# Kernel optimization log

Measured on AMD Instinct MI355X. Metric: run time of the kernel, lower is better.

Reference implementation:

```python
import jax, jax.numpy as jnp
import numpy as np

EPS = 1e-5

def _bn(x, g, b, m, v):
    # eval-mode batchnorm, NCHW, per-channel params
    inv = g / jnp.sqrt(v + EPS)
    return x * inv[None, :, None, None] + (b - m * inv)[None, :, None, None]

def setup_inputs() -> dict:
    key = jax.random.key(0)
    ks = jax.random.split(key, 16)
    C = 64
    x = jax.random.normal(ks[0], (8, C, 64, 64), dtype=jnp.float32)
    w1 = jax.random.normal(ks[1], (C, C, 1, 1), dtype=jnp.float32) * 0.1
    w2 = jax.random.normal(ks[2], (C, 1, 3, 3), dtype=jnp.float32) * 0.1
    w3 = jax.random.normal(ks[3], (C, C, 1, 1), dtype=jnp.float32) * 0.1
    def bn_params(k):
        k1, k2, k3, k4 = jax.random.split(k, 4)
        return (jax.random.uniform(k1, (C,)) + 0.5,
                jax.random.normal(k2, (C,)) * 0.1,
                jax.random.normal(k3, (C,)) * 0.1,
                jax.random.uniform(k4, (C,)) + 0.5)
    g1, b1, m1, v1 = bn_params(ks[4])
    g2, b2, m2, v2 = bn_params(ks[5])
    g3, b3, m3, v3 = bn_params(ks[6])
    return {"x": x, "w1": w1, "bn1_g": g1, "bn1_b": b1, "bn1_m": m1, "bn1_v": v1,
            "w2": w2, "bn2_g": g2, "bn2_b": b2, "bn2_m": m2, "bn2_v": v2,
            "w3": w3, "bn3_g": g3, "bn3_b": b3, "bn3_m": m3, "bn3_v": v3}

def reference(x, w1, bn1_g, bn1_b, bn1_m, bn1_v,
              w2, bn2_g, bn2_b, bn2_m, bn2_v,
              w3, bn3_g, bn3_b, bn3_m, bn3_v):
    B, c, h, w = x.shape
    N = h * w
    # conv1 (1x1) + BN + ReLU -> V
    v = jnp.einsum('bchw,oc->bohw', x, w1[:, :, 0, 0])
    v = jax.nn.relu(_bn(v, bn1_g, bn1_b, bn1_m, bn1_v))
    # attention over spatial positions: Q=K=x, single head, dim=c
    Q = x.reshape(B, c, N)          # bdn
    V = v.reshape(B, c, N)          # bdm
    scores = jnp.einsum('bdn,bdm->bnm', Q, Q) / (c ** 0.5)  # [B,N,N]
    prob = jax.nn.softmax(scores, axis=-1)
    out = jnp.einsum('bnm,bdm->bdn', prob, V).reshape(B, c, h, w)
    # depthwise conv + BN + ReLU
    out = jax.lax.conv_general_dilated(
        out, w2, window_strides=(1, 1), padding='SAME',
        dimension_numbers=('NCHW', 'OIHW', 'NCHW'), feature_group_count=c)
    out = jax.nn.relu(_bn(out, bn2_g, bn2_b, bn2_m, bn2_v))
    # pointwise conv + BN
    out = jnp.einsum('bchw,oc->bohw', out, w3[:, :, 0, 0])
    out = _bn(out, bn3_g, bn3_b, bn3_m, bn3_v)
    # residual (stride==1 and in_size==out_size)
    return out + x
```

## Files before the change

### kernel.cpp

```cpp
#include <hip/hip_runtime.h>
#include <stdint.h>

typedef __attribute__((ext_vector_type(8)))  short s16x8;
typedef __attribute__((ext_vector_type(16))) float f32x16;

union CvtI4 { int4 i; s16x8 s; };

__device__ __forceinline__ unsigned f2bf(float f) {
    union { float f; unsigned u; } v; v.f = f;
    return (v.u + 0x7fffu + ((v.u >> 16) & 1u)) >> 16;
}

__global__ __launch_bounds__(256) void k_prep(
    const float* __restrict__ x, const float* __restrict__ w1,
    const float* __restrict__ g1, const float* __restrict__ b1,
    const float* __restrict__ m1, const float* __restrict__ v1,
    unsigned short* __restrict__ xT, unsigned short* __restrict__ vbf)
{
    __shared__ float X[64 * 65];
    const int b    = blockIdx.x >> 7;
    const int n0   = ((blockIdx.x >> 1) & 63) << 6;
    const int half = blockIdx.x & 1;
    const int tid  = threadIdx.x;
    const float QS = 0.42466090014400953f;

    {
        const int r = tid >> 6, nn = tid & 63;
        const float* xb = x + (size_t)b * 262144 + n0 + nn;
#pragma unroll
        for (int cc = 0; cc < 16; ++cc) {
            int c = cc * 4 + r;
            X[c * 65 + nn] = xb[(size_t)c * 4096];
        }
    }
    __syncthreads();

    {
        const int n8 = tid >> 3, c8 = tid & 7;
        const int n = (half << 5) + n8;
        unsigned u[4];
#pragma unroll
        for (int j = 0; j < 4; ++j) {
            unsigned lo = f2bf(X[(c8 * 8 + 2 * j) * 65 + n] * QS);
            unsigned hi = f2bf(X[(c8 * 8 + 2 * j + 1) * 65 + n] * QS);
            u[j] = lo | (hi << 16);
        }
        uint4 pk; pk.x = u[0]; pk.y = u[1]; pk.z = u[2]; pk.w = u[3];
        *(uint4*)(xT + (((size_t)((b << 12) + n0 + n)) << 6) + (c8 << 3)) = pk;
    }

    {
        const int n = tid & 63, og = tid >> 6;
        float rX[64];
#pragma unroll
        for (int c = 0; c < 64; ++c) rX[c] = X[c * 65 + n];
        unsigned short* vb = vbf + (((size_t)(b << 6)) << 12) + n0 + n;
#pragma unroll 2
        for (int oo = 0; oo < 8; ++oo) {
            int o = (half << 5) + og * 8 + oo;
            float inv = g1[o] * rsqrtf(v1[o] + 1e-5f);
            float sh  = b1[o] - m1[o] * inv;
            float acc = 0.f;
#pragma unroll
            for (int c = 0; c < 64; ++c) acc = fmaf(w1[o * 64 + c], rX[c], acc);
            vb[(size_t)o << 12] = (unsigned short)f2bf(fmaxf(fmaf(acc, inv, sh), 0.f));
        }
    }
}

__global__ __launch_bounds__(512) void k_attn(
    const unsigned short* __restrict__ xT, const unsigned short* __restrict__ vbf,
    unsigned short* __restrict__ outO)
{
    __shared__ __align__(16) unsigned short Klds[2][64 * 64];
    __shared__ __align__(16) unsigned short Vlds[2][64 * 64];
    __shared__ __align__(16) unsigned short Plds[2][64 * 64];
    __shared__ float rsLds[4][32];
    __shared__ float denomT[64];

    const int b    = blockIdx.x & 7;
    const int qgrp = blockIdx.x >> 3;
    const int tid  = threadIdx.x;
    const int w = tid >> 6, lane = tid & 63;
    const int l31 = lane & 31, half = lane >> 5;
    const int qbase = qgrp << 6;
    const int T = 64;

    const bool isQK = (w < 4);
    const int wr = isQK ? w : (w - 4);
    const int s = wr & 1;
    const int t = wr >> 1;

    s16x8 Bq[4];
    float rs = 0.f;
    const int kr0 = (tid & 255) >> 3, c4 = tid & 7;
    const int kr1 = kr0 + 32;
    const size_t kOff0 = (((size_t)((b << 12) + kr0)) << 6) + (c4 << 3);
    const size_t kOff1 = (((size_t)((b << 12) + kr1)) << 6) + (c4 << 3);
    const int kx0 = (c4 ^ (kr0 & 7)) << 3, kx1 = (c4 ^ (kr1 & 7)) << 3;
    const size_t vOff0 = (((size_t)((b << 6) + kr0)) << 12) + (c4 << 3);
    const size_t vOff1 = (((size_t)((b << 6) + kr1)) << 12) + (c4 << 3);

    int4 kpre0, kpre1, vpre0, vpre1;

    f32x16 O = {0.f,0.f,0.f,0.f,0.f,0.f,0.f,0.f,0.f,0.f,0.f,0.f,0.f,0.f,0.f,0.f};

    if (isQK) {
        const unsigned short* qr = xT +
            (((size_t)((b << 12) + qbase + (t << 5) + l31)) << 6) + (half << 3);
#pragma unroll
        for (int kk = 0; kk < 4; ++kk) {
            CvtI4 c; c.i = *(const int4*)(qr + (kk << 4));
            Bq[kk] = c.s;
        }
        {
            int4 a0 = *(const int4*)(xT + kOff0);
            int4 a1 = *(const int4*)(xT + kOff1);
            *(int4*)(Klds[0] + (kr0 << 6) + kx0) = a0;
            *(int4*)(Klds[0] + (kr1 << 6) + kx1) = a1;
            a0 = *(const int4*)(xT + kOff0 + ((size_t)1 << 12));
            a1 = *(const int4*)(xT + kOff1 + ((size_t)1 << 12));
            *(int4*)(Klds[1] + (kr0 << 6) + kx0) = a0;
            *(int4*)(Klds[1] + (kr1 << 6) + kx1) = a1;
            kpre0 = *(const int4*)(xT + kOff0 + ((size_t)2 << 12));
            kpre1 = *(const int4*)(xT + kOff1 + ((size_t)2 << 12));
        }
    } else {
        int4 a0 = *(const int4*)(vbf + vOff0);
        int4 a1 = *(const int4*)(vbf + vOff1);
        *(int4*)(Vlds[0] + (kr0 << 6) + kx0) = a0;
        *(int4*)(Vlds[0] + (kr1 << 6) + kx1) = a1;
        vpre0 = *(const int4*)(vbf + vOff0 + (1 << 6));
        vpre1 = *(const int4*)(vbf + vOff1 + (1 << 6));
    }
    __syncthreads();

    if (isQK) {
        const int km = (s << 5) + l31;
        s16x8 Ak[4];
#pragma unroll
        for (int kk = 0; kk < 4; ++kk)
            Ak[kk] = *(const s16x8*)(Klds[0] + (km << 6) + ((((kk << 1) + half) ^ (km & 7)) << 3));
        f32x16 S = {0.f,0.f,0.f,0.f,0.f,0.f,0.f,0.f,0.f,0.f,0.f,0.f,0.f,0.f,0.f,0.f};
        S = __builtin_amdgcn_mfma_f32_32x32x16_bf16(Ak[0], Bq[0], S, 0, 0, 0);
        S = __builtin_amdgcn_mfma_f32_32x32x16_bf16(Ak[1], Bq[1], S, 0, 0, 0);
        S = __builtin_amdgcn_mfma_f32_32x32x16_bf16(Ak[2], Bq[2], S, 0, 0, 0);
        S = __builtin_amdgcn_mfma_f32_32x32x16_bf16(Ak[3], Bq[3], S, 0, 0, 0);
        const int nrow = (t << 5) + l31;
#pragma unroll
        for (int q = 0; q < 4; ++q) {
            float p0 = __builtin_amdgcn_exp2f(S[4*q+0]);
            float p1 = __builtin_amdgcn_exp2f(S[4*q+1]);
            float p2 = __builtin_amdgcn_exp2f(S[4*q+2]);
            float p3 = __builtin_amdgcn_exp2f(S[4*q+3]);
            rs += (p0 + p1) + (p2 + p3);
            union { float f; unsigned u; } a0, a1, a2, a3;
            a0.f = p0; a1.f = p1; a2.f = p2; a3.f = p3;
            uint2 pk;
            pk.x = __builtin_amdgcn_perm(a1.u + 0x8000u, a0.u + 0x8000u, 0x07060302u);
            pk.y = __builtin_amdgcn_perm(a3.u + 0x8000u, a2.u + 0x8000u, 0x07060302u);
            int c8 = (s << 2) + q;
            *(uint2*)(Plds[0] + (nrow << 6) + ((c8 ^ (nrow & 7)) << 3) + (half << 2)) = pk;
        }
    }
    __syncthreads();

    for (int i = 0; i < T; ++i) {
        if (isQK) {
            *(int4*)(Klds[i & 1] + (kr0 << 6) + kx0) = kpre0;
            *(int4*)(Klds[i & 1] + (kr1 << 6) + kx1) = kpre1;
            {
                size_t tk = (size_t)((i + 3 < T) ? (i + 3) : (T - 1)) << 12;
                kpre0 = *(const int4*)(xT + kOff0 + tk);
                kpre1 = *(const int4*)(xT + kOff1 + tk);
            }
            if (i + 1 < T) {
                const int km = (s << 5) + l31;
                const unsigned short* Kb = Klds[(i + 1) & 1];
                s16x8 Ak[4];
#pragma unroll
                for (int kk = 0; kk < 4; ++kk)
                    Ak[kk] = *(const s16x8*)(Kb + (km << 6) + ((((kk << 1) + half) ^ (km & 7)) << 3));
                f32x16 S = {0.f,0.f,0.f,0.f,0.f,0.f,0.f,0.f,0.f,0.f,0.f,0.f,0.f,0.f,0.f,0.f};
                S = __builtin_amdgcn_mfma_f32_32x32x16_bf16(Ak[0], Bq[0], S, 0, 0, 0);
                S = __builtin_amdgcn_mfma_f32_32x32x16_bf16(Ak[1], Bq[1], S, 0, 0, 0);
                S = __builtin_amdgcn_mfma_f32_32x32x16_bf16(Ak[2], Bq[2], S, 0, 0, 0);
                S = __builtin_amdgcn_mfma_f32_32x32x16_bf16(Ak[3], Bq[3], S, 0, 0, 0);
                const int nrow = (t << 5) + l31;
                unsigned short* Pb = Plds[(i + 1) & 1];
#pragma unroll
                for (int q = 0; q < 4; ++q) {
                    float p0 = __builtin_amdgcn_exp2f(S[4*q+0]);
                    float p1 = __builtin_amdgcn_exp2f(S[4*q+1]);
                    float p2 = __builtin_amdgcn_exp2f(S[4*q+2]);
                    float p3 = __builtin_amdgcn_exp2f(S[4*q+3]);
                    rs += (p0 + p1) + (p2 + p3);
                    union { float f; unsigned u; } a0, a1, a2, a3;
                    a0.f = p0; a1.f = p1; a2.f = p2; a3.f = p3;
                    uint2 pk;
                    pk.x = __builtin_amdgcn_perm(a1.u + 0x8000u, a0.u + 0x8000u, 0x07060302u);
                    pk.y = __builtin_amdgcn_perm(a3.u + 0x8000u, a2.u + 0x8000u, 0x07060302u);
                    int c8 = (s << 2) + q;
                    *(uint2*)(Pb + (nrow << 6) + ((c8 ^ (nrow & 7)) << 3) + (half << 2)) = pk;
                }
            }
        } else {
            *(int4*)(Vlds[(i + 1) & 1] + (kr0 << 6) + kx0) = vpre0;
            *(int4*)(Vlds[(i + 1) & 1] + (kr1 << 6) + kx1) = vpre1;
            {
                int tv = ((i + 2 < T) ? (i + 2) : (T - 1)) << 6;
                vpre0 = *(const int4*)(vbf + vOff0 + tv);
                vpre1 = *(const int4*)(vbf + vOff1 + tv);
            }
            const int nrow = (t << 5) + l31;
            const int drow = (s << 5) + l31;
            const unsigned short* Pb = Plds[i & 1];
            const unsigned short* Vb = Vlds[i & 1];
#pragma unroll
            for (int ks = 0; ks < 4; ++ks) {
                int c = (ks << 1) + half;
                const s16x8 Ap = *(const s16x8*)(Pb + (nrow << 6) + ((c ^ (nrow & 7)) << 3));
                const s16x8 Bv = *(const s16x8*)(Vb + (drow << 6) + ((c ^ (drow & 7)) << 3));
                O = __builtin_amdgcn_mfma_f32_32x32x16_bf16(Ap, Bv, O, 0, 0, 0);
            }
        }
        __syncthreads();
    }

    if (isQK) {
        rs += __shfl_xor(rs, 32);
        if (half == 0) rsLds[w][l31] = rs;
    }
    __syncthreads();
    if (tid < 64) {
        int tt = tid >> 5, n = tid & 31;
        denomT[tid] = rsLds[2 * tt][n] + rsLds[2 * tt + 1][n];
    }
    __syncthreads();

    if (!isQK) {
        const int nb = (b << 12) + qbase;
#pragma unroll
        for (int r = 0; r < 16; ++r) {
            int nl = (r & 3) + ((r >> 2) << 3) + (half << 2);
            int n = (t << 5) + nl;
            float inv = 1.f / denomT[n];
            outO[((size_t)(nb + n) << 6) + (s << 5) + l31] = (unsigned short)f2bf(O[r] * inv);
        }
    }
}

__global__ __launch_bounds__(256) void k_post(
    const unsigned short* __restrict__ Obase,
    const float* __restrict__ x,
    const float* __restrict__ w2,
    const float* __restrict__ g2, const float* __restrict__ b2,
    const float* __restrict__ m2, const float* __restrict__ v2,
    const float* __restrict__ w3,
    const float* __restrict__ g3, const float* __restrict__ b3,
    const float* __restrict__ m3, const float* __restrict__ v3,
    float* __restrict__ out)
{
    __shared__ float W[3][64 * 66];
    __shared__ float T2[64 * 66];

    const int b = blockIdx.x >> 6;
    const int h = blockIdx.x & 63;
    const int tid = threadIdx.x;

#pragma unroll
    for (int r = 0; r < 3; ++r) {
        int hh = h + r - 1;
        if (hh >= 0 && hh <= 63) {
#pragma unroll
            for (int i = 0; i < 2; ++i) {
                int lin = (i << 8) + tid;
                int w = lin >> 3, cg = lin & 7;
                size_t npos = (size_t)((b << 12) + (hh << 6) + w);
                uint4 v = *(const uint4*)(Obase + (npos << 6) + (cg << 3));
                float* Wd = &W[r][w * 66 + (cg << 3)];
                union { float f; unsigned u; } t;
                t.u = v.x << 16;         Wd[0] = t.f;
                t.u = v.x & 0xFFFF0000u; Wd[1] = t.f;
                t.u = v.y << 16;         Wd[2] = t.f;
                t.u = v.y & 0xFFFF0000u; Wd[3] = t.f;
                t.u = v.z << 16;         Wd[4] = t.f;
                t.u = v.z & 0xFFFF0000u; Wd[5] = t.f;
                t.u = v.w << 16;         Wd[6] = t.f;
                t.u = v.w & 0xFFFF0000u; Wd[7] = t.f;
            }
        } else {
#pragma unroll
            for (int i = 0; i < 2; ++i) {
                int lin = (i << 8) + tid;
                float* Wd = &W[r][(lin >> 3) * 66 + ((lin & 7) << 3)];
#pragma unroll
                for (int j = 0; j < 8; ++j) Wd[j] = 0.f;
            }
        }
    }
    __syncthreads();

    const int w = tid & 63, cq = tid >> 6;
    float t16[16];
#pragma unroll
    for (int i = 0; i < 16; ++i) t16[i] = 0.f;

#pragma unroll
    for (int ky = 0; ky < 3; ++ky) {
#pragma unroll
        for (int kx = 0; kx < 3; ++kx) {
            int ww = w + kx - 1;
            if (ww < 0 || ww > 63) continue;
            const int k = ky * 3 + kx;
            const float* Wr = &W[ky][ww * 66 + (cq << 4)];
#pragma unroll
            for (int i = 0; i < 4; ++i) {
                float4 a = *(const float4*)(Wr + (i << 2));
                int c = (cq << 4) + (i << 2);
                t16[i * 4 + 0] = fmaf(w2[(c + 0) * 9 + k], a.x, t16[i * 4 + 0]);
                t16[i * 4 + 1] = fmaf(w2[(c + 1) * 9 + k], a.y, t16[i * 4 + 1]);
                t16[i * 4 + 2] = fmaf(w2[(c + 2) * 9 + k], a.z, t16[i * 4 + 2]);
                t16[i * 4 + 3] = fmaf(w2[(c + 3) * 9 + k], a.w, t16[i * 4 + 3]);
            }
        }
    }
#pragma unroll
    for (int i = 0; i < 16; ++i) {
        int c = (cq << 4) + i;
        float inv = g2[c] * rsqrtf(v2[c] + 1e-5f);
        float sh  = b2[c] - m2[c] * inv;
        T2[w * 66 + c] = fmaxf(fmaf(t16[i], inv, sh), 0.f);
    }
    __syncthreads();

    float rT[64];
#pragma unroll
    for (int c4 = 0; c4 < 16; ++c4)
        *(float4*)&rT[c4 << 2] = *(const float4*)&T2[w * 66 + (c4 << 2)];

    const int hw = (h << 6) + w;
#pragma unroll 2
    for (int oo = 0; oo < 16; ++oo) {
        int o = (cq << 4) + oo;
        float inv = g3[o] * rsqrtf(v3[o] + 1e-5f);
        float sh  = b3[o] - m3[o] * inv;
        float acc = 0.f;
#pragma unroll
        for (int c = 0; c < 64; ++c) acc = fmaf(w3[o * 64 + c], rT[c], acc);
        size_t idx = (((size_t)((b << 6) + o)) << 12) + hw;
        out[idx] = fmaf(acc, inv, sh) + x[idx];
    }
}

extern "C" void kernel_launch(void* const* d_in, const int* in_sizes, int n_in,
                              void* d_out, int out_size, void* d_ws, size_t ws_size,
                              hipStream_t stream)
{
    const float* x  = (const float*)d_in[0];
    const float* w1 = (const float*)d_in[1];
    const float* g1 = (const float*)d_in[2];
    const float* b1 = (const float*)d_in[3];
    const float* m1 = (const float*)d_in[4];
    const float* v1 = (const float*)d_in[5];
    const float* w2 = (const float*)d_in[6];
    const float* g2 = (const float*)d_in[7];
    const float* b2 = (const float*)d_in[8];
    const float* m2 = (const float*)d_in[9];
    const float* v2 = (const float*)d_in[10];
    const float* w3 = (const float*)d_in[11];
    const float* g3 = (const float*)d_in[12];
    const float* b3 = (const float*)d_in[13];
    const float* m3 = (const float*)d_in[14];
    const float* v3 = (const float*)d_in[15];
    float* out = (float*)d_out;

    unsigned short* xT  = (unsigned short*)d_ws;
    unsigned short* vbf = xT + (size_t)8 * 4096 * 64;
    unsigned short* Obase = (unsigned short*)((char*)d_ws + (8u << 20));

    k_prep<<<1024, 256, 0, stream>>>(x, w1, g1, b1, m1, v1, xT, vbf);
    k_attn<<<512, 512, 0, stream>>>(xT, vbf, Obase);
    k_post<<<512, 256, 0, stream>>>(Obase, x, w2, g2, b2, m2, v2,
                                    w3, g3, b3, m3, v3, out);
}
```

Baseline: 194.5 us.

## Split attention KV tiles across two wave groups, load K/V directly to registers

Replaces the producer/consumer split (4 QK waves, 4 PV waves with K/V staged in LDS) with two symmetric groups of 4 waves that each process alternating KV tiles, doing both QK^T/exp and PV per tile. K and V operands are loaded straight from global memory into registers in MFMA layout, which removes the K/V LDS staging. Partial O accumulators and row sums from the two groups are combined through LDS at the end. The change also adds setprio around MFMA blocks and occupancy hint 4, while keeping one barrier per iteration and making each wave do redundant global loads.

```diff
diff --git a/kernel.cpp b/kernel.cpp
--- a/kernel.cpp
+++ b/kernel.cpp
@@ -68,14 +68,12 @@
     }
 }
 
-__global__ __launch_bounds__(512) void k_attn(
+__global__ __launch_bounds__(512, 4) void k_attn(
     const unsigned short* __restrict__ xT, const unsigned short* __restrict__ vbf,
     unsigned short* __restrict__ outO)
 {
-    __shared__ __align__(16) unsigned short Klds[2][64 * 64];
-    __shared__ __align__(16) unsigned short Vlds[2][64 * 64];
-    __shared__ __align__(16) unsigned short Plds[2][64 * 64];
-    __shared__ float rsLds[4][32];
+    __shared__ __align__(16) unsigned short Plds[2][2][64 * 64];
+    __shared__ float rsLds[8][32];
     __shared__ float denomT[64];
 
     const int b    = blockIdx.x & 7;
@@ -84,28 +82,13 @@
     const int w = tid >> 6, lane = tid & 63;
     const int l31 = lane & 31, half = lane >> 5;
     const int qbase = qgrp << 6;
-    const int T = 64;
-
-    const bool isQK = (w < 4);
-    const int wr = isQK ? w : (w - 4);
-    const int s = wr & 1;
-    const int t = wr >> 1;
+    const int qd = w & 3, par = w >> 2;
+    const int s = qd & 1;
+    const int t = qd >> 1;
+    const int nrow = (t << 5) + l31;
 
     s16x8 Bq[4];
-    float rs = 0.f;
-    const int kr0 = (tid & 255) >> 3, c4 = tid & 7;
-    const int kr1 = kr0 + 32;
-    const size_t kOff0 = (((size_t)((b << 12) + kr0)) << 6) + (c4 << 3);
-    const size_t kOff1 = (((size_t)((b << 12) + kr1)) << 6) + (c4 << 3);
-    const int kx0 = (c4 ^ (kr0 & 7)) << 3, kx1 = (c4 ^ (kr1 & 7)) << 3;
-    const size_t vOff0 = (((size_t)((b << 6) + kr0)) << 12) + (c4 << 3);
-    const size_t vOff1 = (((size_t)((b << 6) + kr1)) << 12) + (c4 << 3);
-
-    int4 kpre0, kpre1, vpre0, vpre1;
-
-    f32x16 O = {0.f,0.f,0.f,0.f,0.f,0.f,0.f,0.f,0.f,0.f,0.f,0.f,0.f,0.f,0.f,0.f};
-
-    if (isQK) {
+    {
         const unsigned short* qr = xT +
             (((size_t)((b << 12) + qbase + (t << 5) + l31)) << 6) + (half << 3);
 #pragma unroll
@@ -113,40 +96,48 @@
             CvtI4 c; c.i = *(const int4*)(qr + (kk << 4));
             Bq[kk] = c.s;
         }
+    }
+
+    const unsigned short* aBase = xT +
+        (((size_t)((b << 12) + (s << 5) + l31)) << 6) + (half << 3);
+    const unsigned short* vBase = vbf +
+        (((size_t)((b << 6) + (s << 5) + l31)) << 12) + (half << 3);
+
+    int4 apre[4], vpre[4];
+    {
+        const int tau = par;
+        const unsigned short* ap = aBase + ((size_t)tau << 12);
+        const unsigned short* vp = vBase + (tau << 6);
+#pragma unroll
+        for (int kk = 0; kk < 4; ++kk) apre[kk] = *(const int4*)(ap + (kk << 4));
+#pragma unroll
+        for (int ks = 0; ks < 4; ++ks) vpre[ks] = *(const int4*)(vp + (ks << 4));
+    }
+
+    f32x16 O = {0.f,0.f,0.f,0.f,0.f,0.f,0.f,0.f,0.f,0.f,0.f,0.f,0.f,0.f,0.f,0.f};
+    float rs = 0.f;
+
+    for (int p = 0; p < 32; ++p) {
+        unsigned short* Pb = Plds[p & 1][par];
+
+        f32x16 S = {0.f,0.f,0.f,0.f,0.f,0.f,0.f,0.f,0.f,0.f,0.f,0.f,0.f,0.f,0.f,0.f};
         {
-            int4 a0 = *(const int4*)(xT + kOff0);
-            int4 a1 = *(const int4*)(xT + kOff1);
-            *(int4*)(Klds[0] + (kr0 << 6) + kx0) = a0;
-            *(int4*)(Klds[0] + (kr1 << 6) + kx1) = a1;
-            a0 = *(const int4*)(xT + kOff0 + ((size_t)1 << 12));
-            a1 = *(const int4*)(xT + kOff1 + ((size_t)1 << 12));
-            *(int4*)(Klds[1] + (kr0 << 6) + kx0) = a0;
-            *(int4*)(Klds[1] + (kr1 << 6) + kx1) = a1;
-            kpre0 = *(const int4*)(xT + kOff0 + ((size_t)2 << 12));
-            kpre1 = *(const int4*)(xT + kOff1 + ((size_t)2 << 12));
-        }
-    } else {
-        int4 a0 = *(const int4*)(vbf + vOff0);
-        int4 a1 = *(const int4*)(vbf + vOff1);
-        *(int4*)(Vlds[0] + (kr0 << 6) + kx0) = a0;
-        *(int4*)(Vlds[0] + (kr1 << 6) + kx1) = a1;
-        vpre0 = *(const int4*)(vbf + vOff0 + (1 << 6));
-        vpre1 = *(const int4*)(vbf + vOff1 + (1 << 6));
-    }
-    __syncthreads();
-
-    if (isQK) {
-        const int km = (s << 5) + l31;
-        s16x8 Ak[4];
-#pragma unroll
-        for (int kk = 0; kk < 4; ++kk)
-            Ak[kk] = *(const s16x8*)(Klds[0] + (km << 6) + ((((kk << 1) + half) ^ (km & 7)) << 3));
-        f32x16 S = {0.f,0.f,0.f,0.f,0.f,0.f,0.f,0.f,0.f,0.f,0.f,0.f,0.f,0.f,0.f,0.f};
-        S = __builtin_amdgcn_mfma_f32_32x32x16_bf16(Ak[0], Bq[0], S, 0, 0, 0);
-        S = __builtin_amdgcn_mfma_f32_32x32x16_bf16(Ak[1], Bq[1], S, 0, 0, 0);
-        S = __builtin_amdgcn_mfma_f32_32x32x16_bf16(Ak[2], Bq[2], S, 0, 0, 0);
-        S = __builtin_amdgcn_mfma_f32_32x32x16_bf16(Ak[3], Bq[3], S, 0, 0, 0);
-        const int nrow = (t << 5) + l31;
+            s16x8 Ak[4];
+#pragma unroll
+            for (int kk = 0; kk < 4; ++kk) { CvtI4 c; c.i = apre[kk]; Ak[kk] = c.s; }
+            __builtin_amdgcn_s_setprio(1);
+            S = __builtin_amdgcn_mfma_f32_32x32x16_bf16(Ak[0], Bq[0], S, 0, 0, 0);
+            S = __builtin_amdgcn_mfma_f32_32x32x16_bf16(Ak[1], Bq[1], S, 0, 0, 0);
+            S = __builtin_amdgcn_mfma_f32_32x32x16_bf16(Ak[2], Bq[2], S, 0, 0, 0);
+            S = __builtin_amdgcn_mfma_f32_32x32x16_bf16(Ak[3], Bq[3], S, 0, 0, 0);
+            __builtin_amdgcn_s_setprio(0);
+        }
+        {
+            const int tn = (p < 31) ? (((p + 1) << 1) + par) : 63;
+            const unsigned short* ap = aBase + ((size_t)tn << 12);
+#pragma unroll
+            for (int kk = 0; kk < 4; ++kk) apre[kk] = *(const int4*)(ap + (kk << 4));
+        }
 #pragma unroll
         for (int q = 0; q < 4; ++q) {
             float p0 = __builtin_amdgcn_exp2f(S[4*q+0]);
@@ -160,92 +151,58 @@
             pk.x = __builtin_amdgcn_perm(a1.u + 0x8000u, a0.u + 0x8000u, 0x07060302u);
             pk.y = __builtin_amdgcn_perm(a3.u + 0x8000u, a2.u + 0x8000u, 0x07060302u);
             int c8 = (s << 2) + q;
-            *(uint2*)(Plds[0] + (nrow << 6) + ((c8 ^ (nrow & 7)) << 3) + (half << 2)) = pk;
-        }
-    }
-    __syncthreads();
-
-    for (int i = 0; i < T; ++i) {
-        if (isQK) {
-            *(int4*)(Klds[i & 1] + (kr0 << 6) + kx0) = kpre0;
-            *(int4*)(Klds[i & 1] + (kr1 << 6) + kx1) = kpre1;
-            {
-                size_t tk = (size_t)((i + 3 < T) ? (i + 3) : (T - 1)) << 12;
-                kpre0 = *(const int4*)(xT + kOff0 + tk);
-                kpre1 = *(const int4*)(xT + kOff1 + tk);
-            }
-            if (i + 1 < T) {
-                const int km = (s << 5) + l31;
-                const unsigned short* Kb = Klds[(i + 1) & 1];
-                s16x8 Ak[4];
-#pragma unroll
-                for (int kk = 0; kk < 4; ++kk)
-                    Ak[kk] = *(const s16x8*)(Kb + (km << 6) + ((((kk << 1) + half) ^ (km & 7)) << 3));
-                f32x16 S = {0.f,0.f,0.f,0.f,0.f,0.f,0.f,0.f,0.f,0.f,0.f,0.f,0.f,0.f,0.f,0.f};
-                S = __builtin_amdgcn_mfma_f32_32x32x16_bf16(Ak[0], Bq[0], S, 0, 0, 0);
-                S = __builtin_amdgcn_mfma_f32_32x32x16_bf16(Ak[1], Bq[1], S, 0, 0, 0);
-                S = __builtin_amdgcn_mfma_f32_32x32x16_bf16(Ak[2], Bq[2], S, 0, 0, 0);
-                S = __builtin_amdgcn_mfma_f32_32x32x16_bf16(Ak[3], Bq[3], S, 0, 0, 0);
-                const int nrow = (t << 5) + l31;
-                unsigned short* Pb = Plds[(i + 1) & 1];
-#pragma unroll
-                for (int q = 0; q < 4; ++q) {
-                    float p0 = __builtin_amdgcn_exp2f(S[4*q+0]);
-                    float p1 = __builtin_amdgcn_exp2f(S[4*q+1]);
-                    float p2 = __builtin_amdgcn_exp2f(S[4*q+2]);
-                    float p3 = __builtin_amdgcn_exp2f(S[4*q+3]);
-                    rs += (p0 + p1) + (p2 + p3);
-                    union { float f; unsigned u; } a0, a1, a2, a3;
-                    a0.f = p0; a1.f = p1; a2.f = p2; a3.f = p3;
-                    uint2 pk;
-                    pk.x = __builtin_amdgcn_perm(a1.u + 0x8000u, a0.u + 0x8000u, 0x07060302u);
-                    pk.y = __builtin_amdgcn_perm(a3.u + 0x8000u, a2.u + 0x8000u, 0x07060302u);
-                    int c8 = (s << 2) + q;
-                    *(uint2*)(Pb + (nrow << 6) + ((c8 ^ (nrow & 7)) << 3) + (half << 2)) = pk;
-                }
-            }
-        } else {
-            *(int4*)(Vlds[(i + 1) & 1] + (kr0 << 6) + kx0) = vpre0;
-            *(int4*)(Vlds[(i + 1) & 1] + (kr1 << 6) + kx1) = vpre1;
-            {
-                int tv = ((i + 2 < T) ? (i + 2) : (T - 1)) << 6;
-                vpre0 = *(const int4*)(vbf + vOff0 + tv);
-                vpre1 = *(const int4*)(vbf + vOff1 + tv);
-            }
-            const int nrow = (t << 5) + l31;
-            const int drow = (s << 5) + l31;
-            const unsigned short* Pb = Plds[i & 1];
-            const unsigned short* Vb = Vlds[i & 1];
+            *(uint2*)(Pb + (nrow << 6) + ((c8 ^ (nrow & 7)) << 3) + (half << 2)) = pk;
+        }
+
+        __syncthreads();
+
+        {
+            __builtin_amdgcn_s_setprio(1);
 #pragma unroll
             for (int ks = 0; ks < 4; ++ks) {
                 int c = (ks << 1) + half;
                 const s16x8 Ap = *(const s16x8*)(Pb + (nrow << 6) + ((c ^ (nrow & 7)) << 3));
-                const s16x8 Bv = *(const s16x8*)(Vb + (drow << 6) + ((c ^ (drow & 7)) << 3));
-                O = __builtin_amdgcn_mfma_f32_32x32x16_bf16(Ap, Bv, O, 0, 0, 0);
+                CvtI4 cv; cv.i = vpre[ks];
+                O = __builtin_amdgcn_mfma_f32_32x32x16_bf16(Ap, cv.s, O, 0, 0, 0);
             }
-        }
-        __syncthreads();
-    }
-
-    if (isQK) {
-        rs += __shfl_xor(rs, 32);
-        if (half == 0) rsLds[w][l31] = rs;
-    }
-    __syncthreads();
+            __builtin_amdgcn_s_setprio(0);
+        }
+        {
+            const int tn = (p < 31) ? (((p + 1) << 1) + par) : 63;
+            const unsigned short* vp = vBase + (tn << 6);
+#pragma unroll
+            for (int ks = 0; ks < 4; ++ks) vpre[ks] = *(const int4*)(vp + (ks << 4));
+        }
+    }
+
+    rs += __shfl_xor(rs, 32);
+    if (half == 0) rsLds[w][l31] = rs;
+    __syncthreads();
+
     if (tid < 64) {
         int tt = tid >> 5, n = tid & 31;
-        denomT[tid] = rsLds[2 * tt][n] + rsLds[2 * tt + 1][n];
-    }
-    __syncthreads();
-
-    if (!isQK) {
+        denomT[tid] = (rsLds[2*tt][n] + rsLds[2*tt+1][n]) +
+                      (rsLds[4+2*tt][n] + rsLds[5+2*tt][n]);
+    }
+    float* Ox = (float*)&Plds[0][0][0];
+    if (par == 1) {
+#pragma unroll
+        for (int r = 0; r < 16; ++r) {
+            int row = (r & 3) + ((r >> 2) << 3) + (half << 2);
+            Ox[(qd << 10) + (row << 5) + l31] = O[r];
+        }
+    }
+    __syncthreads();
+
+    if (par == 0) {
         const int nb = (b << 12) + qbase;
 #pragma unroll
         for (int r = 0; r < 16; ++r) {
-            int nl = (r & 3) + ((r >> 2) << 3) + (half << 2);
-            int n = (t << 5) + nl;
+            int row = (r & 3) + ((r >> 2) << 3) + (half << 2);
+            float o = O[r] + Ox[(qd << 10) + (row << 5) + l31];
+            int n = (t << 5) + row;
             float inv = 1.f / denomT[n];
-            outO[((size_t)(nb + n) << 6) + (s << 5) + l31] = (unsigned short)f2bf(O[r] * inv);
+            outO[((size_t)(nb + n) << 6) + (s << 5) + l31] = (unsigned short)f2bf(o * inv);
         }
     }
 }
```

Measured after the change: 257.2 us. 32.3% more time.
